# Performance work log

Hardware: AMD Instinct MI355X
Metric: run time of the kernel (lower is better)

The kernel has to match this reference:

```python
import jax, jax.numpy as jnp
import numpy as np
import math

N_EMBD = 1024
N_HEAD = 16
B, T = 4, 2048

def setup_inputs() -> dict:
    key = jax.random.key(0)
    k1, k2, k3, k4, k5 = jax.random.split(key, 5)
    C = N_EMBD
    scale_in = 1.0 / math.sqrt(C)
    x = jax.random.normal(k1, (B, T, C), dtype=jnp.float32)
    W_attn = jax.random.normal(k2, (C, 3 * C), dtype=jnp.float32) * scale_in
    b_attn = jax.random.normal(k3, (3 * C,), dtype=jnp.float32) * 0.02
    W_proj = jax.random.normal(k4, (C, C), dtype=jnp.float32) * scale_in
    b_proj = jax.random.normal(k5, (C,), dtype=jnp.float32) * 0.02
    attention_mask = jnp.ones((B, T), dtype=jnp.int32)
    return {"x": x, "W_attn": W_attn, "b_attn": b_attn,
            "W_proj": W_proj, "b_proj": b_proj,
            "attention_mask": attention_mask}

def reference(x, W_attn, b_attn, W_proj, b_proj, attention_mask):
    Bx, Tx, C = x.shape
    H = N_HEAD
    D = C // H
    qkv = x @ W_attn + b_attn                      # [B,T,3C]
    q, k, v = jnp.split(qkv, 3, axis=-1)
    # [B,H,T,D]
    q = q.reshape(Bx, Tx, H, D).transpose(0, 2, 1, 3)
    k = k.reshape(Bx, Tx, H, D).transpose(0, 2, 1, 3)
    v = v.reshape(Bx, Tx, H, D).transpose(0, 2, 1, 3)
    att = jnp.einsum('bhqd,bhkd->bhqk', q, k) * (1.0 / math.sqrt(D))
    causal = jnp.tril(jnp.ones((Tx, Tx), dtype=bool))  # [T,T]
    neg_inf = jnp.float32(-jnp.inf)
    att = jnp.where(causal[None, None, :, :], att, neg_inf)
    pad = (attention_mask != 0)[:, None, None, :]      # [B,1,1,T]
    att = jnp.where(pad, att, neg_inf)
    att = jax.nn.softmax(att, axis=-1)
    y = jnp.einsum('bhqk,bhkd->bhqd', att, v)          # [B,H,T,D]
    y = y.transpose(0, 2, 1, 3).reshape(Bx, Tx, C)
    y = y @ W_proj + b_proj
    return y
```

## Files before the change

kernel.cpp:

```cpp
#include <hip/hip_runtime.h>
#include <hip/hip_bf16.h>
#include <stdint.h>

#define B_ 4
#define T_ 2048
#define C_ 1024
#define H_ 16
#define D_ 64
#define BH_ (B_*H_)
#define M_ (B_*T_)

typedef __attribute__((ext_vector_type(8))) short short8;
typedef __attribute__((ext_vector_type(4))) float f32x4;
typedef __attribute__((ext_vector_type(16))) float f32x16;

#if __has_builtin(__builtin_amdgcn_exp2f)
#define EXP2(x) __builtin_amdgcn_exp2f(x)
#else
#define EXP2(x) exp2f(x)
#endif

#define QSCALE 0.18033688011112043f

__device__ __forceinline__ unsigned short f2bf(float f) {
  union { float f; unsigned int u; } v; v.f = f;
  unsigned int r = v.u + 0x7FFFu + ((v.u >> 16) & 1u);
  return (unsigned short)(r >> 16);
}

__device__ __forceinline__ unsigned int cvtpk_bf16(float lo, float hi) {
  unsigned int r;
  asm("v_cvt_pk_bf16_f32 %0, %1, %2" : "=v"(r) : "v"(lo), "v"(hi));
  return r;
}

__device__ __forceinline__ void gload_lds16(const void* g, void* l) {
  __builtin_amdgcn_global_load_lds(
      (__attribute__((address_space(1))) void*)g,
      (__attribute__((address_space(3))) void*)l, 16, 0, 0);
}

__global__ __launch_bounds__(256) void k_cvt(const float* __restrict__ in,
                                             unsigned short* __restrict__ out, int n) {
  int i = (blockIdx.x * 256 + threadIdx.x) * 4;
  if (i >= n) return;
  float4 v = *reinterpret_cast<const float4*>(in + i);
  union { unsigned short u[4]; unsigned long long ll; } o;
  o.u[0] = f2bf(v.x); o.u[1] = f2bf(v.y); o.u[2] = f2bf(v.z); o.u[3] = f2bf(v.w);
  *reinterpret_cast<unsigned long long*>(out + i) = o.ll;
}

__global__ __launch_bounds__(256) void k_tr(const float* __restrict__ W,
                                            unsigned short* __restrict__ Wt, int K, int N) {
  __shared__ float t[32][33];
  int n0 = blockIdx.x * 32, k0 = blockIdx.y * 32;
  int tx = threadIdx.x, ty = threadIdx.y;
  #pragma unroll
  for (int j = 0; j < 4; j++)
    t[ty + j*8][tx] = W[(size_t)(k0 + ty + j*8) * N + n0 + tx];
  __syncthreads();
  #pragma unroll
  for (int j = 0; j < 4; j++)
    Wt[(size_t)(n0 + ty + j*8) * K + k0 + tx] = f2bf(t[tx][ty + j*8]);
}

template<int QKV>
__global__ __launch_bounds__(512) void k_gemm8(const unsigned short* __restrict__ A,
                                               const unsigned short* __restrict__ Bt,
                                               const float* __restrict__ bias,
                                               void* __restrict__ outp, int N, int K) {
  __shared__ __align__(16) unsigned short Al[2][256*64];
  __shared__ __align__(16) unsigned short Bl[2][128*64];

  const int tid = threadIdx.x;
  const int lane = tid & 63, wv = tid >> 6;
  const int lg = lane >> 4, lr = lane & 15;
  const int wm = wv >> 2, wn = wv & 3;

  const int nwg = gridDim.x * gridDim.y;
  const int l = blockIdx.y * gridDim.x + blockIdx.x;
  const int wg = (l & 7) * (nwg >> 3) + (l >> 3);
  const int m0 = (wg / gridDim.x) * 256;
  const int n0 = (wg % gridDim.x) * 128;

  const int NT = K >> 6;

  auto stageA = [&](int s, int t, int u) {
    int row = u*64 + (tid >> 3), g = tid & 7;
    gload_lds16(A + (size_t)(m0 + row) * K + t*64 + (g ^ (row & 7)) * 8,
                (char*)Al + s*32768 + u*8192 + tid*16);
  };
  auto stageB = [&](int s, int t, int u) {
    int row = u*64 + (tid >> 3), g = tid & 7;
    gload_lds16(Bt + (size_t)(n0 + row) * K + t*64 + (g ^ (row & 7)) * 8,
                (char*)Bl + s*16384 + u*8192 + tid*16);
  };

  f32x4 acc[8][2];
  #pragma unroll
  for (int i = 0; i < 8; ++i)
    #pragma unroll
    for (int j = 0; j < 2; ++j) acc[i][j] = (f32x4){0.f, 0.f, 0.f, 0.f};

  stageB(0,0,0); stageB(0,0,1); stageA(0,0,0); stageA(0,0,2);
  stageA(0,0,1); stageA(0,0,3);
  asm volatile("s_waitcnt vmcnt(2)" ::: "memory");
  __builtin_amdgcn_s_barrier();

#define GPH(MhC, READB, STAGE, WAITE)  do {                                     \
    short8 af_[4][2];                                                           \
    _Pragma("unroll") for (int mf = 0; mf < 4; ++mf) {                          \
      int rA = wm*128 + (MhC)*64 + mf*16 + lr;                                  \
      int r7 = rA & 7;                                                          \
      af_[mf][0] = *(const short8*)(Asb + rA*128 + ((lg      ^ r7) << 4));      \
      af_[mf][1] = *(const short8*)(Asb + rA*128 + (((4|lg) ^ r7) << 4));       \
    }                                                                           \
    if (READB) {                                                                \
      _Pragma("unroll") for (int nf = 0; nf < 2; ++nf) {                        \
        int rB = wn*32 + nf*16 + lr;                                            \
        int r7 = rB & 7;                                                        \
        bf_[nf][0] = *(const short8*)(Bsb + rB*128 + ((lg      ^ r7) << 4));    \
        bf_[nf][1] = *(const short8*)(Bsb + rB*128 + (((4|lg) ^ r7) << 4));     \
      }                                                                         \
    }                                                                           \
    STAGE;                                                                      \
    __builtin_amdgcn_s_barrier();                                               \
    asm volatile("s_waitcnt lgkmcnt(0)" ::: "memory");                          \
    __builtin_amdgcn_sched_barrier(0);                                          \
    __builtin_amdgcn_s_setprio(1);                                              \
    _Pragma("unroll") for (int kh = 0; kh < 2; ++kh)                            \
      _Pragma("unroll") for (int mf = 0; mf < 4; ++mf)                          \
        _Pragma("unroll") for (int nf = 0; nf < 2; ++nf)                        \
          acc[(MhC)*4+mf][nf] = __builtin_amdgcn_mfma_f32_16x16x32_bf16(        \
              af_[mf][kh], bf_[nf][kh], acc[(MhC)*4+mf][nf], 0, 0, 0);          \
    __builtin_amdgcn_s_setprio(0);                                              \
    WAITE;                                                                      \
    __builtin_amdgcn_s_barrier();                                               \
  } while (0)

  for (int t = 0; t < NT; ++t) {
    const char* Asb = (const char*)Al + (t & 1) * 32768;
    const char* Bsb = (const char*)Bl + (t & 1) * 16384;
    const int s1 = (t & 1) ^ 1;
    const bool p1 = (t + 1 < NT);
    short8 bf_[2][2];
    GPH(0, 1,
        if (p1) { stageB(s1,t+1,0); stageB(s1,t+1,1); stageA(s1,t+1,0); stageA(s1,t+1,2); },
        if (p1) { asm volatile("s_waitcnt vmcnt(4)" ::: "memory"); }
        else    { asm volatile("s_waitcnt vmcnt(0)" ::: "memory"); });
    GPH(1, 0,
        if (p1) { stageA(s1,t+1,1); stageA(s1,t+1,3); },
        if (p1) { asm volatile("s_waitcnt vmcnt(2)" ::: "memory"); }
        else    { asm volatile("s_waitcnt vmcnt(0)" ::: "memory"); });
  }
#undef GPH

  if (QKV) {
    unsigned short* qb = (unsigned short*)outp;
    const size_t SZ = (size_t)BH_ * T_ * D_;
    #pragma unroll
    for (int i8 = 0; i8 < 8; ++i8) {
      int mb = m0 + wm*128 + i8*16 + lg*4;
      #pragma unroll
      for (int nf = 0; nf < 2; ++nf) {
        int n = n0 + wn*32 + nf*16 + lr;
        float bv = bias[n];
        int which = n >> 10, c = n & 1023, h = c >> 6, d = c & 63;
        unsigned short* base = qb + (size_t)which * SZ;
        #pragma unroll
        for (int r = 0; r < 4; ++r) {
          int m = mb + r;
          int bb2 = m >> 11, tt = m & 2047;
          float y = acc[i8][nf][r] + bv;
          if (which == 0) y *= QSCALE;
          base[((size_t)(bb2*H_ + h)*T_ + tt)*D_ + d] = f2bf(y);
        }
      }
    }
  } else {
    float* out = (float*)outp;
    #pragma unroll
    for (int i8 = 0; i8 < 8; ++i8) {
      int mb = m0 + wm*128 + i8*16 + lg*4;
      #pragma unroll
      for (int nf = 0; nf < 2; ++nf) {
        int n = n0 + wn*32 + nf*16 + lr;
        float bv = bias[n];
        #pragma unroll
        for (int r = 0; r < 4; ++r)
          out[(size_t)(mb + r)*N + n] = acc[i8][nf][r] + bv;
      }
    }
  }
}

__global__ __launch_bounds__(256, 3) void k_attn4(const unsigned short* __restrict__ Qb,
                                                  const unsigned short* __restrict__ Kb,
                                                  const unsigned short* __restrict__ Vb,
                                                  const int* __restrict__ amask,
                                                  unsigned short* __restrict__ Yb) {
  __shared__ __align__(16) char pool[32768];

  const int l = blockIdx.y * 16 + blockIdx.x;
  const int local = l >> 3;
  const int tq = 15 - (local >> 3);
  const int bh = (l & 7) * 8 + (local & 7);
  const int bb = bh >> 4, hh = bh & 15;

  const int tid = threadIdx.x;
  const int lane = tid & 63, w = tid >> 6;
  const int hi = lane >> 5, l31 = lane & 31;

  const unsigned short* Qh = Qb + (size_t)bh * (T_*D_);
  const unsigned short* Kh = Kb + (size_t)bh * (T_*D_);
  const unsigned short* Vh = Vb + (size_t)bh * (T_*D_);

  const int kvp = tid & 31, d0v = (tid >> 5) * 8;

  auto stage_load = [&](int i, int b, short8& sv0, short8& sv1, int& nm) {
    const int kv0 = i << 6;
    char* base = pool + b * 16384;
    #pragma unroll
    for (int s = 0; s < 2; ++s) {
      int gi = tid + s * 256;
      int row = gi >> 3, gc = gi & 7;
      gload_lds16(Kh + (size_t)(kv0 + row)*D_ + (gc ^ (row & 7)) * 8, base + gi * 16);
    }
    int kv = kv0 + 2 * kvp;
    sv0 = *reinterpret_cast<const short8*>(Vh + (size_t)kv*D_ + d0v);
    sv1 = *reinterpret_cast<const short8*>(Vh + (size_t)(kv + 1)*D_ + d0v);
    nm = amask[bb*T_ + kv0 + lane];
  };
  auto stage_write = [&](int b, short8 sv0, short8 sv1) {
    unsigned int* vt = (unsigned int*)(pool + b * 16384 + 8192);
    #pragma unroll
    for (int jj = 0; jj < 8; ++jj) {
      int d = d0v + jj;
      unsigned int wd = (unsigned short)sv0[jj] | ((unsigned int)(unsigned short)sv1[jj] << 16);
      vt[d * 32 + (kvp ^ ((d & 7) << 2))] = wd;
    }
  };

  const int nT = 2 * tq + 2;
  const int qbase = tq << 7;
  const int qw = qbase + w * 32;
  const int q  = qw + l31;

  short8 qf[4];
  #pragma unroll
  for (int dt = 0; dt < 4; ++dt)
    qf[dt] = *reinterpret_cast<const short8*>(Qh + (size_t)q*D_ + dt*16 + hi*8);

  f32x16 o0, o1;
  #pragma unroll
  for (int r = 0; r < 16; ++r) { o0[r] = 0.f; o1[r] = 0.f; }
  float mr = -1e30f, ls = 0.f;

  short8 sv0, sv1; int cm;
  stage_load(0, 0, sv0, sv1, cm);
  stage_write(0, sv0, sv1);
  __syncthreads();

  for (int i = 0; i < nT; ++i) {
    const int b = i & 1;
    const bool pf = (i + 1 < nT);
    short8 nv0, nv1; int nm = 0;
    if (pf) stage_load(i + 1, b ^ 1, nv0, nv1, nm);
    const int kv0 = i << 6;

    if (kv0 <= qw + 31) {
      const unsigned short* Klb = (const unsigned short*)(pool + b * 16384);
      const char* Vtb = pool + b * 16384 + 8192;

      f32x16 st0, st1;
      #pragma unroll
      for (int r = 0; r < 16; ++r) { st0[r] = 0.f; st1[r] = 0.f; }
      __builtin_amdgcn_s_setprio(1);
      #pragma unroll
      for (int dt = 0; dt < 4; ++dt) {
        int gg = dt * 2 + hi;
        int ra = l31;
        short8 kf0 = *reinterpret_cast<const short8*>(Klb + ra*64 + (gg ^ (ra & 7)) * 8);
        st0 = __builtin_amdgcn_mfma_f32_32x32x16_bf16(kf0, qf[dt], st0, 0, 0, 0);
        int rb = 32 + l31;
        short8 kf1 = *reinterpret_cast<const short8*>(Klb + rb*64 + (gg ^ (rb & 7)) * 8);
        st1 = __builtin_amdgcn_mfma_f32_32x32x16_bf16(kf1, qf[dt], st1, 0, 0, 0);
      }
      __builtin_amdgcn_s_setprio(0);

      if (kv0 + 63 > qw) {
        #pragma unroll
        for (int r = 0; r < 16; ++r) {
          int kvl = (r & 3) + 8 * (r >> 2) + 4 * hi;
          if (kv0 + kvl      > q) st0[r] = -1e30f;
          if (kv0 + 32 + kvl > q) st1[r] = -1e30f;
        }
      }
      unsigned long long mb = __ballot(cm != 0);
      if (mb != ~0ull) {
        #pragma unroll
        for (int r = 0; r < 16; ++r) {
          int kvl = (r & 3) + 8 * (r >> 2) + 4 * hi;
          if (!((mb >> kvl) & 1))        st0[r] = -1e30f;
          if (!((mb >> (kvl + 32)) & 1)) st1[r] = -1e30f;
        }
      }

      float mm[8];
      #pragma unroll
      for (int r = 0; r < 8; ++r)
        mm[r] = fmaxf(fmaxf(st0[r], st0[r + 8]), fmaxf(st1[r], st1[r + 8]));
      #pragma unroll
      for (int s = 4; s > 0; s >>= 1)
        #pragma unroll
        for (int r = 0; r < s; ++r) mm[r] = fmaxf(mm[r], mm[r + s]);
      float mo = fmaxf(mm[0], __shfl_xor(mm[0], 32));
      if (!__all(mo <= mr + 8.0f)) {
        float mnew = fmaxf(mr, mo);
        float corr = EXP2(mr - mnew);
        ls *= corr;
        #pragma unroll
        for (int r = 0; r < 16; ++r) { o0[r] *= corr; o1[r] *= corr; }
        mr = mnew;
      }
      float rp[8];
      #pragma unroll
      for (int r = 0; r < 8; ++r) rp[r] = 0.f;
      #pragma unroll
      for (int r = 0; r < 16; ++r) {
        st0[r] = EXP2(st0[r] - mr); rp[r & 7]       += st0[r];
        st1[r] = EXP2(st1[r] - mr); rp[(r & 7) ^ 4] += st1[r];
      }
      float rs = ((rp[0] + rp[1]) + (rp[2] + rp[3])) + ((rp[4] + rp[5]) + (rp[6] + rp[7]));
      rs += __shfl_xor(rs, 32);
      ls += rs;

      unsigned int pw[2][4][2];
      #pragma unroll
      for (int a = 0; a < 4; ++a) {
        pw[0][a][0] = cvtpk_bf16(st0[4*a],   st0[4*a+1]);
        pw[0][a][1] = cvtpk_bf16(st0[4*a+2], st0[4*a+3]);
        pw[1][a][0] = cvtpk_bf16(st1[4*a],   st1[4*a+1]);
        pw[1][a][1] = cvtpk_bf16(st1[4*a+2], st1[4*a+3]);
      }

      #pragma unroll
      for (int kt = 0; kt < 4; ++kt) {
        const int t = kt >> 1, h2 = kt & 1;
        unsigned int send0 = hi ? pw[t][2*h2][0]   : pw[t][2*h2+1][0];
        unsigned int send1 = hi ? pw[t][2*h2][1]   : pw[t][2*h2+1][1];
        unsigned int own0  = hi ? pw[t][2*h2+1][0] : pw[t][2*h2][0];
        unsigned int own1  = hi ? pw[t][2*h2+1][1] : pw[t][2*h2][1];
        unsigned int recv0 = __shfl_xor(send0, 32);
        unsigned int recv1 = __shfl_xor(send1, 32);
        union { unsigned int u[4]; short8 v; } pf2;
        pf2.u[0] = hi ? recv0 : own0;
        pf2.u[1] = hi ? recv1 : own1;
        pf2.u[2] = hi ? own0  : recv0;
        pf2.u[3] = hi ? own1  : recv1;
        int gg = kt * 2 + hi;
        int dA = l31;
        short8 vf0 = *reinterpret_cast<const short8*>(Vtb + dA*128 + ((gg ^ (dA & 7)) * 16));
        int dB = 32 + l31;
        short8 vf1 = *reinterpret_cast<const short8*>(Vtb + dB*128 + ((gg ^ (dB & 7)) * 16));
        __builtin_amdgcn_s_setprio(1);
        o0 = __builtin_amdgcn_mfma_f32_32x32x16_bf16(vf0, pf2.v, o0, 0, 0, 0);
        o1 = __builtin_amdgcn_mfma_f32_32x32x16_bf16(vf1, pf2.v, o1, 0, 0, 0);
        __builtin_amdgcn_s_setprio(0);
      }
    }
    if (pf) { stage_write(b ^ 1, nv0, nv1); cm = nm; }
    __syncthreads();
  }

  float inv = 1.0f / ls;
  size_t rowbase = ((size_t)bb*T_ + q)*C_ + hh*D_;
  #pragma unroll
  for (int a = 0; a < 4; ++a) {
    union { unsigned short h[4]; unsigned long long ll; } y0, y1;
    #pragma unroll
    for (int bq = 0; bq < 4; ++bq) {
      int r = 4*a + bq;
      y0.h[bq] = f2bf(o0[r] * inv);
      y1.h[bq] = f2bf(o1[r] * inv);
    }
    int d0o = 8*a + 4*hi;
    *reinterpret_cast<unsigned long long*>(Yb + rowbase + d0o)      = y0.ll;
    *reinterpret_cast<unsigned long long*>(Yb + rowbase + 32 + d0o) = y1.ll;
  }
}

extern "C" void kernel_launch(void* const* d_in, const int* in_sizes, int n_in,
                              void* d_out, int out_size, void* d_ws, size_t ws_size,
                              hipStream_t stream) {
  const float* x      = (const float*)d_in[0];
  const float* W_attn = (const float*)d_in[1];
  const float* b_attn = (const float*)d_in[2];
  const float* W_proj = (const float*)d_in[3];
  const float* b_proj = (const float*)d_in[4];
  const int*   amask  = (const int*)d_in[5];
  float* out = (float*)d_out;

  char* ws = (char*)d_ws;
  size_t off = 0;
  auto alloc = [&](size_t bytes) { char* p = ws + off; off += (bytes + 255) & ~(size_t)255; return p; };
  unsigned short* xb   = (unsigned short*)alloc((size_t)M_ * C_ * 2);
  unsigned short* Wta  = (unsigned short*)alloc((size_t)3 * C_ * C_ * 2);
  unsigned short* Wtp  = (unsigned short*)alloc((size_t)C_ * C_ * 2);
  unsigned short* qkvb = (unsigned short*)alloc((size_t)3 * BH_ * T_ * D_ * 2);
  unsigned short* Yb   = (unsigned short*)alloc((size_t)M_ * C_ * 2);

  k_cvt<<<(M_ * C_) / 1024, 256, 0, stream>>>(x, xb, M_ * C_);
  k_tr<<<dim3(3*C_/32, C_/32), dim3(32, 8), 0, stream>>>(W_attn, Wta, C_, 3*C_);
  k_tr<<<dim3(C_/32,  C_/32),  dim3(32, 8), 0, stream>>>(W_proj, Wtp, C_, C_);

  k_gemm8<1><<<dim3(3*C_/128, M_/256), 512, 0, stream>>>(xb, Wta, b_attn, qkvb, 3*C_, C_);

  unsigned short* Qb = qkvb;
  unsigned short* Kb = qkvb + (size_t)BH_ * T_ * D_;
  unsigned short* Vb = qkvb + 2 * (size_t)BH_ * T_ * D_;
  k_attn4<<<dim3(16, BH_), 256, 0, stream>>>(Qb, Kb, Vb, amask, Yb);

  k_gemm8<0><<<dim3(C_/128, M_/256), 512, 0, stream>>>(Yb, Wtp, b_proj, out, C_, C_);
}
```

Measured before the change: 180.6 us.

## Double KV tile to 128 rows per iteration in attention kernel

The attention loop now stages 128 K/V rows per iteration instead of 64. The LDS pool doubles to 64KB, the transposed-V swizzle is widened, and occupancy drops from 3 to 2 blocks per CU. The aim is to halve the number of barriers and loop iterations and to amortise softmax bookkeeping over more MFMAs. The cost is lower occupancy, more registers, and no per-warp skip of fully masked tiles: every warp now computes the whole diagonal tile and relies on masking.

```diff
diff --git a/kernel.cpp b/kernel.cpp
--- a/kernel.cpp
+++ b/kernel.cpp
@@ -194,12 +194,12 @@
   }
 }
 
-__global__ __launch_bounds__(256, 3) void k_attn4(const unsigned short* __restrict__ Qb,
+__global__ __launch_bounds__(256, 2) void k_attn4(const unsigned short* __restrict__ Qb,
                                                   const unsigned short* __restrict__ Kb,
                                                   const unsigned short* __restrict__ Vb,
                                                   const int* __restrict__ amask,
                                                   unsigned short* __restrict__ Yb) {
-  __shared__ __align__(16) char pool[32768];
+  __shared__ __align__(16) char pool[65536];
 
   const int l = blockIdx.y * 16 + blockIdx.x;
   const int local = l >> 3;
@@ -215,33 +215,39 @@
   const unsigned short* Kh = Kb + (size_t)bh * (T_*D_);
   const unsigned short* Vh = Vb + (size_t)bh * (T_*D_);
 
-  const int kvp = tid & 31, d0v = (tid >> 5) * 8;
-
-  auto stage_load = [&](int i, int b, short8& sv0, short8& sv1, int& nm) {
-    const int kv0 = i << 6;
-    char* base = pool + b * 16384;
-    #pragma unroll
-    for (int s = 0; s < 2; ++s) {
+  const int vp = tid & 63, vdb = tid >> 6;
+
+  auto stage_load = [&](int i, int b, short8 (&sv)[4], int& nm0, int& nm1) {
+    const int kv0 = i << 7;
+    char* base = pool + b * 32768;
+    #pragma unroll
+    for (int s = 0; s < 4; ++s) {
       int gi = tid + s * 256;
       int row = gi >> 3, gc = gi & 7;
       gload_lds16(Kh + (size_t)(kv0 + row)*D_ + (gc ^ (row & 7)) * 8, base + gi * 16);
     }
-    int kv = kv0 + 2 * kvp;
-    sv0 = *reinterpret_cast<const short8*>(Vh + (size_t)kv*D_ + d0v);
-    sv1 = *reinterpret_cast<const short8*>(Vh + (size_t)(kv + 1)*D_ + d0v);
-    nm = amask[bb*T_ + kv0 + lane];
+    const unsigned short* vsrc = Vh + (size_t)(kv0 + 2*vp)*D_ + vdb*16;
+    sv[0] = *reinterpret_cast<const short8*>(vsrc);
+    sv[1] = *reinterpret_cast<const short8*>(vsrc + 8);
+    sv[2] = *reinterpret_cast<const short8*>(vsrc + D_);
+    sv[3] = *reinterpret_cast<const short8*>(vsrc + D_ + 8);
+    nm0 = amask[bb*T_ + kv0 + lane];
+    nm1 = amask[bb*T_ + kv0 + 64 + lane];
   };
-  auto stage_write = [&](int b, short8 sv0, short8 sv1) {
-    unsigned int* vt = (unsigned int*)(pool + b * 16384 + 8192);
-    #pragma unroll
-    for (int jj = 0; jj < 8; ++jj) {
-      int d = d0v + jj;
-      unsigned int wd = (unsigned short)sv0[jj] | ((unsigned int)(unsigned short)sv1[jj] << 16);
-      vt[d * 32 + (kvp ^ ((d & 7) << 2))] = wd;
+  auto stage_write = [&](int b, const short8 (&sv)[4]) {
+    unsigned int* vt = (unsigned int*)(pool + b * 32768 + 16384);
+    #pragma unroll
+    for (int j = 0; j < 16; ++j) {
+      int d = vdb*16 + j;
+      unsigned short lo = (unsigned short)((j < 8) ? sv[0][j] : sv[1][j-8]);
+      unsigned short hv = (unsigned short)((j < 8) ? sv[2][j] : sv[3][j-8]);
+      unsigned int wd = lo | ((unsigned int)hv << 16);
+      int pcol = (((vp >> 2) ^ (d & 15)) << 2) | (vp & 3);
+      vt[d * 64 + pcol] = wd;
     }
   };
 
-  const int nT = 2 * tq + 2;
+  const int nT = tq + 1;
   const int qbase = tq << 7;
   const int qw = qbase + w * 32;
   const int q  = qw + l31;
@@ -256,120 +262,130 @@
   for (int r = 0; r < 16; ++r) { o0[r] = 0.f; o1[r] = 0.f; }
   float mr = -1e30f, ls = 0.f;
 
-  short8 sv0, sv1; int cm;
-  stage_load(0, 0, sv0, sv1, cm);
-  stage_write(0, sv0, sv1);
+  short8 sv[4]; int cm0, cm1;
+  stage_load(0, 0, sv, cm0, cm1);
+  stage_write(0, sv);
   __syncthreads();
 
   for (int i = 0; i < nT; ++i) {
     const int b = i & 1;
     const bool pf = (i + 1 < nT);
-    short8 nv0, nv1; int nm = 0;
-    if (pf) stage_load(i + 1, b ^ 1, nv0, nv1, nm);
-    const int kv0 = i << 6;
-
-    if (kv0 <= qw + 31) {
-      const unsigned short* Klb = (const unsigned short*)(pool + b * 16384);
-      const char* Vtb = pool + b * 16384 + 8192;
-
-      f32x16 st0, st1;
-      #pragma unroll
-      for (int r = 0; r < 16; ++r) { st0[r] = 0.f; st1[r] = 0.f; }
-      __builtin_amdgcn_s_setprio(1);
-      #pragma unroll
-      for (int dt = 0; dt < 4; ++dt) {
-        int gg = dt * 2 + hi;
-        int ra = l31;
-        short8 kf0 = *reinterpret_cast<const short8*>(Klb + ra*64 + (gg ^ (ra & 7)) * 8);
-        st0 = __builtin_amdgcn_mfma_f32_32x32x16_bf16(kf0, qf[dt], st0, 0, 0, 0);
-        int rb = 32 + l31;
-        short8 kf1 = *reinterpret_cast<const short8*>(Klb + rb*64 + (gg ^ (rb & 7)) * 8);
-        st1 = __builtin_amdgcn_mfma_f32_32x32x16_bf16(kf1, qf[dt], st1, 0, 0, 0);
-      }
-      __builtin_amdgcn_s_setprio(0);
-
-      if (kv0 + 63 > qw) {
+    short8 nv[4]; int nm0 = 0, nm1 = 0;
+    if (pf) stage_load(i + 1, b ^ 1, nv, nm0, nm1);
+    const int kv0 = i << 7;
+
+    const unsigned short* Klb = (const unsigned short*)(pool + b * 32768);
+    const char* Vtb = pool + b * 32768 + 16384;
+
+    f32x16 st[4];
+    #pragma unroll
+    for (int tl = 0; tl < 4; ++tl)
+      #pragma unroll
+      for (int r = 0; r < 16; ++r) st[tl][r] = 0.f;
+    __builtin_amdgcn_s_setprio(1);
+    #pragma unroll
+    for (int dt = 0; dt < 4; ++dt) {
+      int gg = dt * 2 + hi;
+      #pragma unroll
+      for (int tl = 0; tl < 4; ++tl) {
+        int ra = tl*32 + l31;
+        short8 kf = *reinterpret_cast<const short8*>(Klb + ra*64 + ((gg ^ (ra & 7)) * 8));
+        st[tl] = __builtin_amdgcn_mfma_f32_32x32x16_bf16(kf, qf[dt], st[tl], 0, 0, 0);
+      }
+    }
+    __builtin_amdgcn_s_setprio(0);
+
+    if (kv0 + 127 > qw) {
+      #pragma unroll
+      for (int tl = 0; tl < 4; ++tl)
+        #pragma unroll
+        for (int r = 0; r < 16; ++r) {
+          int kvl = tl*32 + (r & 3) + 8 * (r >> 2) + 4 * hi;
+          if (kv0 + kvl > q) st[tl][r] = -1e30f;
+        }
+    }
+    unsigned long long mb0 = __ballot(cm0 != 0);
+    unsigned long long mb1 = __ballot(cm1 != 0);
+    if ((mb0 & mb1) != ~0ull) {
+      #pragma unroll
+      for (int tl = 0; tl < 4; ++tl) {
+        unsigned long long mb = (tl < 2) ? mb0 : mb1;
+        int sh0 = (tl & 1) * 32;
         #pragma unroll
         for (int r = 0; r < 16; ++r) {
           int kvl = (r & 3) + 8 * (r >> 2) + 4 * hi;
-          if (kv0 + kvl      > q) st0[r] = -1e30f;
-          if (kv0 + 32 + kvl > q) st1[r] = -1e30f;
+          if (!((mb >> (kvl + sh0)) & 1)) st[tl][r] = -1e30f;
         }
       }
-      unsigned long long mb = __ballot(cm != 0);
-      if (mb != ~0ull) {
-        #pragma unroll
-        for (int r = 0; r < 16; ++r) {
-          int kvl = (r & 3) + 8 * (r >> 2) + 4 * hi;
-          if (!((mb >> kvl) & 1))        st0[r] = -1e30f;
-          if (!((mb >> (kvl + 32)) & 1)) st1[r] = -1e30f;
-        }
-      }
-
-      float mm[8];
-      #pragma unroll
-      for (int r = 0; r < 8; ++r)
-        mm[r] = fmaxf(fmaxf(st0[r], st0[r + 8]), fmaxf(st1[r], st1[r + 8]));
-      #pragma unroll
-      for (int s = 4; s > 0; s >>= 1)
-        #pragma unroll
-        for (int r = 0; r < s; ++r) mm[r] = fmaxf(mm[r], mm[r + s]);
-      float mo = fmaxf(mm[0], __shfl_xor(mm[0], 32));
-      if (!__all(mo <= mr + 8.0f)) {
-        float mnew = fmaxf(mr, mo);
-        float corr = EXP2(mr - mnew);
-        ls *= corr;
-        #pragma unroll
-        for (int r = 0; r < 16; ++r) { o0[r] *= corr; o1[r] *= corr; }
-        mr = mnew;
-      }
-      float rp[8];
-      #pragma unroll
-      for (int r = 0; r < 8; ++r) rp[r] = 0.f;
+    }
+
+    float mm[8];
+    #pragma unroll
+    for (int r = 0; r < 8; ++r)
+      mm[r] = fmaxf(fmaxf(fmaxf(st[0][r], st[0][r+8]), fmaxf(st[1][r], st[1][r+8])),
+                    fmaxf(fmaxf(st[2][r], st[2][r+8]), fmaxf(st[3][r], st[3][r+8])));
+    #pragma unroll
+    for (int s = 4; s > 0; s >>= 1)
+      #pragma unroll
+      for (int r = 0; r < s; ++r) mm[r] = fmaxf(mm[r], mm[r + s]);
+    float mo = fmaxf(mm[0], __shfl_xor(mm[0], 32));
+    if (!__all(mo <= mr + 8.0f)) {
+      float mnew = fmaxf(mr, mo);
+      float corr = EXP2(mr - mnew);
+      ls *= corr;
+      #pragma unroll
+      for (int r = 0; r < 16; ++r) { o0[r] *= corr; o1[r] *= corr; }
+      mr = mnew;
+    }
+    float rp[8];
+    #pragma unroll
+    for (int r = 0; r < 8; ++r) rp[r] = 0.f;
+    #pragma unroll
+    for (int tl = 0; tl < 4; ++tl)
       #pragma unroll
       for (int r = 0; r < 16; ++r) {
-        st0[r] = EXP2(st0[r] - mr); rp[r & 7]       += st0[r];
-        st1[r] = EXP2(st1[r] - mr); rp[(r & 7) ^ 4] += st1[r];
-      }
-      float rs = ((rp[0] + rp[1]) + (rp[2] + rp[3])) + ((rp[4] + rp[5]) + (rp[6] + rp[7]));
-      rs += __shfl_xor(rs, 32);
-      ls += rs;
-
-      unsigned int pw[2][4][2];
+        st[tl][r] = EXP2(st[tl][r] - mr);
+        rp[r & 7] += st[tl][r];
+      }
+    float rs = ((rp[0] + rp[1]) + (rp[2] + rp[3])) + ((rp[4] + rp[5]) + (rp[6] + rp[7]));
+    rs += __shfl_xor(rs, 32);
+    ls += rs;
+
+    unsigned int pw[4][4][2];
+    #pragma unroll
+    for (int tl = 0; tl < 4; ++tl)
       #pragma unroll
       for (int a = 0; a < 4; ++a) {
-        pw[0][a][0] = cvtpk_bf16(st0[4*a],   st0[4*a+1]);
-        pw[0][a][1] = cvtpk_bf16(st0[4*a+2], st0[4*a+3]);
-        pw[1][a][0] = cvtpk_bf16(st1[4*a],   st1[4*a+1]);
-        pw[1][a][1] = cvtpk_bf16(st1[4*a+2], st1[4*a+3]);
-      }
-
-      #pragma unroll
-      for (int kt = 0; kt < 4; ++kt) {
-        const int t = kt >> 1, h2 = kt & 1;
-        unsigned int send0 = hi ? pw[t][2*h2][0]   : pw[t][2*h2+1][0];
-        unsigned int send1 = hi ? pw[t][2*h2][1]   : pw[t][2*h2+1][1];
-        unsigned int own0  = hi ? pw[t][2*h2+1][0] : pw[t][2*h2][0];
-        unsigned int own1  = hi ? pw[t][2*h2+1][1] : pw[t][2*h2][1];
-        unsigned int recv0 = __shfl_xor(send0, 32);
-        unsigned int recv1 = __shfl_xor(send1, 32);
-        union { unsigned int u[4]; short8 v; } pf2;
-        pf2.u[0] = hi ? recv0 : own0;
-        pf2.u[1] = hi ? recv1 : own1;
-        pf2.u[2] = hi ? own0  : recv0;
-        pf2.u[3] = hi ? own1  : recv1;
-        int gg = kt * 2 + hi;
-        int dA = l31;
-        short8 vf0 = *reinterpret_cast<const short8*>(Vtb + dA*128 + ((gg ^ (dA & 7)) * 16));
-        int dB = 32 + l31;
-        short8 vf1 = *reinterpret_cast<const short8*>(Vtb + dB*128 + ((gg ^ (dB & 7)) * 16));
-        __builtin_amdgcn_s_setprio(1);
-        o0 = __builtin_amdgcn_mfma_f32_32x32x16_bf16(vf0, pf2.v, o0, 0, 0, 0);
-        o1 = __builtin_amdgcn_mfma_f32_32x32x16_bf16(vf1, pf2.v, o1, 0, 0, 0);
-        __builtin_amdgcn_s_setprio(0);
-      }
-    }
-    if (pf) { stage_write(b ^ 1, nv0, nv1); cm = nm; }
+        pw[tl][a][0] = cvtpk_bf16(st[tl][4*a],   st[tl][4*a+1]);
+        pw[tl][a][1] = cvtpk_bf16(st[tl][4*a+2], st[tl][4*a+3]);
+      }
+
+    #pragma unroll
+    for (int kt = 0; kt < 8; ++kt) {
+      const int t = kt >> 1, h2 = kt & 1;
+      unsigned int send0 = hi ? pw[t][2*h2][0]   : pw[t][2*h2+1][0];
+      unsigned int send1 = hi ? pw[t][2*h2][1]   : pw[t][2*h2+1][1];
+      unsigned int own0  = hi ? pw[t][2*h2+1][0] : pw[t][2*h2][0];
+      unsigned int own1  = hi ? pw[t][2*h2+1][1] : pw[t][2*h2][1];
+      unsigned int recv0 = __shfl_xor(send0, 32);
+      unsigned int recv1 = __shfl_xor(send1, 32);
+      union { unsigned int u[4]; short8 v; } pf2;
+      pf2.u[0] = hi ? recv0 : own0;
+      pf2.u[1] = hi ? recv1 : own1;
+      pf2.u[2] = hi ? own0  : recv0;
+      pf2.u[3] = hi ? own1  : recv1;
+      int gg = kt * 2 + hi;
+      int dA = l31;
+      short8 vf0 = *reinterpret_cast<const short8*>(Vtb + dA*256 + ((gg ^ (dA & 15)) * 16));
+      int dB = 32 + l31;
+      short8 vf1 = *reinterpret_cast<const short8*>(Vtb + dB*256 + ((gg ^ (dB & 15)) * 16));
+      __builtin_amdgcn_s_setprio(1);
+      o0 = __builtin_amdgcn_mfma_f32_32x32x16_bf16(vf0, pf2.v, o0, 0, 0, 0);
+      o1 = __builtin_amdgcn_mfma_f32_32x32x16_bf16(vf1, pf2.v, o1, 0, 0, 0);
+      __builtin_amdgcn_s_setprio(0);
+    }
+
+    if (pf) { stage_write(b ^ 1, nv); cm0 = nm0; cm1 = nm1; }
     __syncthreads();
   }
 
```

After: 172.2 us. -4.7%, faster.
